# Kernel tuning notes

Measured on AMD Instinct MI355X. Metric: run time of the kernel, lower is better.

## Reference

```python
import jax, jax.numpy as jnp
import numpy as np

N_NODES = 100000
N_EDGES = 3200000
N_GRAPHS = 256
VOCAB = 1500


def gcn_conv(x, edge_index, W, b, n_nodes):
    # x: [N, Fin], edge_index: [2, E] (row=source, col=target)
    h = x @ W  # [N, Fout]
    loops = jnp.arange(n_nodes, dtype=edge_index.dtype)
    row = jnp.concatenate([edge_index[0], loops])
    col = jnp.concatenate([edge_index[1], loops])
    # symmetric normalization with self-loops (PyG GCNConv default)
    deg = jax.ops.segment_sum(jnp.ones_like(col, dtype=h.dtype), col,
                              num_segments=n_nodes)
    dinv = jnp.where(deg > 0, jax.lax.rsqrt(deg), 0.0)
    norm = dinv[row] * dinv[col]  # [E+N]
    msg = h[row] * norm[:, None]  # gather + scale
    out = jax.ops.segment_sum(msg, col, num_segments=n_nodes)  # scatter-add
    return out + b


def setup_inputs() -> dict:
    key = jax.random.key(0)
    k = jax.random.split(key, 8)
    x_ids = jax.random.randint(k[0], (N_NODES,), 0, VOCAB)
    edge_index = jax.random.randint(k[1], (2, N_EDGES), 0, N_NODES)
    batch = jnp.sort(jax.random.randint(k[2], (N_NODES,), 0, N_GRAPHS))
    emb_table = jax.random.normal(k[3], (VOCAB, 16), dtype=jnp.float32)
    W1 = jax.random.normal(k[4], (16, 32), dtype=jnp.float32) * (1.0 / np.sqrt(16))
    b1 = jnp.zeros((32,), dtype=jnp.float32)
    W2 = jax.random.normal(k[5], (32, 41), dtype=jnp.float32) * (1.0 / np.sqrt(32))
    b2 = jnp.zeros((41,), dtype=jnp.float32)
    return {"x_ids": x_ids, "edge_index": edge_index, "batch": batch,
            "emb_table": emb_table, "W1": W1, "b1": b1, "W2": W2, "b2": b2}


def reference(x_ids, edge_index, batch, emb_table, W1, b1, W2, b2):
    x = emb_table[x_ids]                      # embedding lookup [N,16]
    x = gcn_conv(x, edge_index, W1, b1, N_NODES)
    x = jax.nn.relu(x)                        # dropout is identity in eval
    x = gcn_conv(x, edge_index, W2, b2, N_NODES)
    # scatter_add pooling over graphs in batch
    return jax.ops.segment_sum(x, batch, num_segments=N_GRAPHS)  # [G,41]
```

## Files before the change

### kernel.cpp

```cpp
#include <hip/hip_runtime.h>


constexpr int EPB = 16384;
constexpr int BSH = 8;
constexpr int BKTN = 1 << BSH;
constexpr int CAP = 10240;

__device__ inline unsigned short f2bf(float x) {
  unsigned u = __float_as_uint(x);
  u += 0x7FFF + ((u >> 16) & 1);
  return (unsigned short)(u >> 16);
}
__device__ inline float bf2f(unsigned short h) {
  return __uint_as_float((unsigned)h << 16);
}
__device__ inline unsigned pk(float a, float b) {
  return (unsigned)f2bf(a) | ((unsigned)f2bf(b) << 16);
}
__device__ __forceinline__ void add8(float acc[8], uint4 v) {
  acc[0] += bf2f(v.x & 0xFFFF); acc[1] += bf2f(v.x >> 16);
  acc[2] += bf2f(v.y & 0xFFFF); acc[3] += bf2f(v.y >> 16);
  acc[4] += bf2f(v.z & 0xFFFF); acc[5] += bf2f(v.z >> 16);
  acc[6] += bf2f(v.w & 0xFFFF); acc[7] += bf2f(v.w >> 16);
}

__device__ __forceinline__ void gather8(const unsigned short* __restrict__ base,
                                        const int* list, int st, int dg,
                                        float acc[8]) {
  int j = 0;
  for (; j + 4 <= dg; j += 4) {
    int r0 = list[st + j], r1 = list[st + j + 1];
    int r2 = list[st + j + 2], r3 = list[st + j + 3];
    uint4 v0 = *(const uint4*)(base + (size_t)r0 * 16);
    uint4 v1 = *(const uint4*)(base + (size_t)r1 * 16);
    uint4 v2 = *(const uint4*)(base + (size_t)r2 * 16);
    uint4 v3 = *(const uint4*)(base + (size_t)r3 * 16);
    add8(acc, v0); add8(acc, v1); add8(acc, v2); add8(acc, v3);
  }
  for (; j < dg; ++j)
    add8(acc, *(const uint4*)(base + (size_t)list[st + j] * 16));
}

__device__ __forceinline__ int swz(int b, int nblkp) {
  return (b & 7) * (nblkp >> 3) + (b >> 3);
}

__global__ __launch_bounds__(1024) void k_scatter(const int* __restrict__ row,
                                                  const int* __restrict__ col, int E,
                                                  int nbkt, int nblkp,
                                                  int* __restrict__ cursor,
                                                  int* __restrict__ staging) {
  __shared__ int sbuf[EPB];
  __shared__ int cnt[512], sc[512], cur[512], gbase[512];
  int tid = threadIdx.x;
  int lane = tid & 63, wv = tid >> 6;
  int blk = swz(blockIdx.x, nblkp);
  if (tid < 512) cnt[tid] = 0;
  __syncthreads();
  int e0 = blk * EPB, e1 = min(E, e0 + EPB);
  for (int e = e0 + tid; e < e1; e += 1024)
    atomicAdd(&cnt[col[e] >> BSH], 1);
  __syncthreads();
  if (tid < 512) {
    int c = cnt[tid];
    sc[tid] = c;
    gbase[tid] = c ? atomicAdd(&cursor[tid], c) : 0;
  }
  __syncthreads();
  for (int o = 1; o < 512; o <<= 1) {
    int u = (tid < 512 && tid >= o) ? sc[tid - o] : 0;
    __syncthreads();
    if (tid < 512) sc[tid] += u;
    __syncthreads();
  }
  if (tid < 512) { int st = sc[tid] - cnt[tid]; sc[tid] = st; cur[tid] = st; }
  __syncthreads();
  for (int e = e0 + tid; e < e1; e += 1024) {
    int c = col[e];
    int b = c >> BSH;
    int pos = atomicAdd(&cur[b], 1);
    sbuf[pos] = (row[e] << BSH) | (c & (BKTN - 1));
  }
  __syncthreads();
  for (int b = wv; b < nbkt; b += 16) {
    int lbeg = sc[b], lcnt = cnt[b];
    int gb = gbase[b];
    int lim = CAP - gb;
    if (lcnt > lim) lcnt = lim > 0 ? lim : 0;
    int g = b * CAP + gb;
    for (int j = lane; j < lcnt; j += 64)
      staging[g + j] = sbuf[lbeg + j];
  }
}

__global__ __launch_bounds__(512) void k_build(const int* __restrict__ staging,
                                               const int* __restrict__ cursor,
                                               const int* __restrict__ x_ids,
                                               const float* __restrict__ emb,
                                               int N, int nbkt,
                                               int* __restrict__ col_ptr,
                                               int* __restrict__ endp,
                                               float* __restrict__ dinv,
                                               unsigned short* __restrict__ ag1,
                                               int* __restrict__ edge_row) {
  __shared__ int list[CAP];
  __shared__ int cnt[BKTN], sc[BKTN], lcur[BKTN];
  int tid = threadIdx.x, b = blockIdx.x;
  int beg = b * CAP;
  int total = min(cursor[b], CAP);
  int end = beg + total;
  if (tid < BKTN) cnt[tid] = 0;
  __syncthreads();
  for (int i = beg + tid; i < end; i += 512)
    atomicAdd(&cnt[staging[i] & (BKTN - 1)], 1);
  __syncthreads();
  if (tid < BKTN) sc[tid] = cnt[tid];
  __syncthreads();
  for (int o = 1; o < BKTN; o <<= 1) {
    int u = (tid < BKTN && tid >= o) ? sc[tid - o] : 0;
    __syncthreads();
    if (tid < BKTN) sc[tid] += u;
    __syncthreads();
  }
  if (tid < BKTN) {
    int excl = sc[tid] - cnt[tid];
    sc[tid] = excl;
    lcur[tid] = excl;
    int node = (b << BSH) + tid;
    if (node < N) col_ptr[node] = beg + excl;
  }
  if (tid == 0) {
    endp[b] = end;
    if (b == nbkt - 1) col_ptr[N] = end;
  }
  __syncthreads();
  for (int i = beg + tid; i < end; i += 512) {
    int p = staging[i];
    list[atomicAdd(&lcur[p & (BKTN - 1)], 1)] = p >> BSH;
  }
  __syncthreads();
  for (int i = beg + tid; i < end; i += 512)
    edge_row[i] = list[i - beg];
  int nloc = tid >> 1, half = tid & 1;
  int node = (b << BSH) + nloc;
  if (node < N) {
    float d = rsqrtf((float)(cnt[nloc] + 1));
    if (half == 0) dinv[node] = d;
    const float* er = emb + (size_t)x_ids[node] * 16 + half * 8;
    float4 e0 = *(const float4*)(er);
    float4 e1 = *(const float4*)(er + 4);
    uint4 o;
    o.x = pk(e0.x * d, e0.y * d); o.y = pk(e0.z * d, e0.w * d);
    o.z = pk(e1.x * d, e1.y * d); o.w = pk(e1.z * d, e1.w * d);
    *(uint4*)(ag1 + (size_t)node * 16 + half * 8) = o;
  }
}

__global__ __launch_bounds__(512) void k_fuse1(const unsigned short* __restrict__ ag1,
                                               const int* __restrict__ edge_row,
                                               const int* __restrict__ col_ptr,
                                               const int* __restrict__ endp,
                                               const float* __restrict__ dinv,
                                               const float* __restrict__ W1,
                                               const float* __restrict__ b1, int N,
                                               unsigned short* __restrict__ y1g) {
  __shared__ int list[CAP];
  __shared__ float W[512];
  __shared__ float bb[32];
  int tid = threadIdx.x, b = blockIdx.x;
  W[tid] = W1[tid];
  if (tid < 32) bb[tid] = b1[tid];
  int nloc = tid >> 1, half = tid & 1;
  int node = (b << BSH) + nloc;
  bool valid = node < N;
  int beg = b * CAP;
  int end = endp[b];
  int ms = 0, me = 0;
  float acc[8];
  if (valid) {
    ms = col_ptr[node];
    me = (nloc == BKTN - 1) ? end : col_ptr[node + 1];
    uint4 v = *(const uint4*)(ag1 + (size_t)node * 16 + half * 8);
    acc[0] = bf2f(v.x & 0xFFFF); acc[1] = bf2f(v.x >> 16);
    acc[2] = bf2f(v.y & 0xFFFF); acc[3] = bf2f(v.y >> 16);
    acc[4] = bf2f(v.z & 0xFFFF); acc[5] = bf2f(v.z >> 16);
    acc[6] = bf2f(v.w & 0xFFFF); acc[7] = bf2f(v.w >> 16);
  } else {
#pragma unroll
    for (int k = 0; k < 8; ++k) acc[k] = 0.f;
  }
  for (int cbeg = beg; cbeg < end; cbeg += CAP) {
    int cend = min(end, cbeg + CAP);
    __syncthreads();
    for (int i = cbeg + tid; i < cend; i += 512) list[i - cbeg] = edge_row[i];
    __syncthreads();
    if (valid) {
      int st = max(ms, cbeg), en = min(me, cend);
      if (en > st) gather8(ag1 + half * 8, list, st - cbeg, en - st, acc);
    }
  }
  if (!valid) return;
  float d = dinv[node];
  float sx[8], xo[8];
#pragma unroll
  for (int k = 0; k < 8; ++k) sx[k] = acc[k] * d;
#pragma unroll
  for (int k = 0; k < 8; ++k) xo[k] = __shfl_xor(sx[k], 1);
  float x[16];
  if (half == 0) {
#pragma unroll
    for (int k = 0; k < 8; ++k) { x[k] = sx[k]; x[8 + k] = xo[k]; }
  } else {
#pragma unroll
    for (int k = 0; k < 8; ++k) { x[k] = xo[k]; x[8 + k] = sx[k]; }
  }
  int j0 = half * 16;
  float a[16];
#pragma unroll
  for (int j = 0; j < 16; ++j) a[j] = bb[j0 + j];
#pragma unroll
  for (int k = 0; k < 16; ++k) {
    float xv = x[k];
#pragma unroll
    for (int j = 0; j < 16; ++j) a[j] += xv * W[k * 32 + j0 + j];
  }
#pragma unroll
  for (int j = 0; j < 16; ++j) a[j] = fmaxf(a[j], 0.f) * d;
  uint4 o0 = {pk(a[0], a[1]), pk(a[2], a[3]), pk(a[4], a[5]), pk(a[6], a[7])};
  uint4 o1 = {pk(a[8], a[9]), pk(a[10], a[11]), pk(a[12], a[13]), pk(a[14], a[15])};
  unsigned short* yp = y1g + (size_t)half * N * 16 + (size_t)node * 16;
  *(uint4*)(yp) = o0;
  *(uint4*)(yp + 8) = o1;
}

__global__ __launch_bounds__(512) void k_fuse2(const unsigned short* __restrict__ y1g,
                                               const int* __restrict__ edge_row,
                                               const int* __restrict__ col_ptr,
                                               const int* __restrict__ endp,
                                               const float* __restrict__ dinv,
                                               const int* __restrict__ batch, int N,
                                               int nbkt, float* __restrict__ P) {
  __shared__ int list[CAP];
  __shared__ float pool[8 * 16];
  int bx = blockIdx.x;
  int plane = (bx >> 2) & 1;
  int b = (bx >> 3) * 4 + (bx & 3);
  if (b >= nbkt) return;
  const unsigned short* __restrict__ y1p = y1g + (size_t)plane * N * 16;
  int pofs = plane << 4;
  int tid = threadIdx.x;
  int nloc = tid >> 1, half = tid & 1;
  int node = (b << BSH) + nloc;
  bool valid = node < N;
  int beg = b * CAP;
  int end = endp[b];
  int ms = 0, me = 0;
  float acc[8];
  if (valid) {
    ms = col_ptr[node];
    me = (nloc == BKTN - 1) ? end : col_ptr[node + 1];
    uint4 v = *(const uint4*)(y1p + (size_t)node * 16 + half * 8);
    acc[0] = bf2f(v.x & 0xFFFF); acc[1] = bf2f(v.x >> 16);
    acc[2] = bf2f(v.y & 0xFFFF); acc[3] = bf2f(v.y >> 16);
    acc[4] = bf2f(v.z & 0xFFFF); acc[5] = bf2f(v.z >> 16);
    acc[6] = bf2f(v.w & 0xFFFF); acc[7] = bf2f(v.w >> 16);
  } else {
#pragma unroll
    for (int k = 0; k < 8; ++k) acc[k] = 0.f;
  }
  for (int cbeg = beg; cbeg < end; cbeg += CAP) {
    int cend = min(end, cbeg + CAP);
    __syncthreads();
    for (int i = cbeg + tid; i < cend; i += 512) list[i - cbeg] = edge_row[i];
    __syncthreads();
    if (valid) {
      int st = max(ms, cbeg), en = min(me, cend);
      if (en > st) gather8(y1p + half * 8, list, st - cbeg, en - st, acc);
    }
  }
  int myg = -1;
  if (valid) {
    float d = dinv[node];
#pragma unroll
    for (int k = 0; k < 8; ++k) acc[k] *= d;
    myg = batch[node];
  }
  int g0 = batch[b << BSH];
  int g1 = batch[min((b << BSH) + BKTN - 1, N - 1)];
  for (int clo = g0; clo <= g1; clo += 8) {
    for (int j = tid; j < 8 * 16; j += 512) pool[j] = 0.f;
    __syncthreads();
    if (myg >= clo && myg < clo + 8) {
      float* pp = pool + (myg - clo) * 16 + half * 8;
#pragma unroll
      for (int k = 0; k < 8; ++k) atomicAdd(pp + k, acc[k]);
    }
    __syncthreads();
    int ng = min(8, g1 - clo + 1);
    for (int j = tid; j < ng * 16; j += 512)
      atomicAdd(&P[(size_t)(clo + (j >> 4)) * 32 + pofs + (j & 15)], pool[j]);
    __syncthreads();
  }
}

__global__ __launch_bounds__(64) void k_final(const float* __restrict__ P,
                                              const int* __restrict__ batch, int N,
                                              const float* __restrict__ W2,
                                              const float* __restrict__ b2,
                                              float* __restrict__ out) {
  __shared__ float pr[32];
  __shared__ int se[2];
  int g = blockIdx.x, tid = threadIdx.x;
  if (tid < 2) {
    int v = g + tid;
    int lo = 0, hi = N;
    while (lo < hi) {
      int mid = (lo + hi) >> 1;
      if (batch[mid] < v) lo = mid + 1; else hi = mid;
    }
    se[tid] = lo;
  }
  if (tid < 32) pr[tid] = P[(size_t)g * 32 + tid];
  __syncthreads();
  if (tid < 41) {
    float o = (float)(se[1] - se[0]) * b2[tid];
#pragma unroll
    for (int k = 0; k < 32; ++k) o += pr[k] * W2[k * 41 + tid];
    out[(size_t)g * 41 + tid] = o;
  }
}

extern "C" void kernel_launch(void* const* d_in, const int* in_sizes, int n_in,
                              void* d_out, int out_size, void* d_ws, size_t ws_size,
                              hipStream_t stream) {
  const int* x_ids = (const int*)d_in[0];
  const int* edge_index = (const int*)d_in[1];
  const int* batch = (const int*)d_in[2];
  const float* emb = (const float*)d_in[3];
  const float* W1 = (const float*)d_in[4];
  const float* b1 = (const float*)d_in[5];
  const float* W2 = (const float*)d_in[6];
  const float* b2 = (const float*)d_in[7];
  float* out = (float*)d_out;

  const int N = in_sizes[0];
  const int E = in_sizes[1] / 2;
  const int G = out_size / 41;
  const int* row = edge_index;
  const int* col = edge_index + E;

  const int nbkt = (N + BKTN - 1) >> BSH;
  int nblk = (E + EPB - 1) / EPB;
  const int nblkp = (nblk + 7) & ~7;
  const int nbkt4 = (nbkt + 3) & ~3;

  char* ws = (char*)d_ws;
  size_t woff = 0;
  auto alloc = [&](size_t bytes) -> char* {
    char* p = ws + woff;
    woff += (bytes + 255) & ~(size_t)255;
    return p;
  };
  int* staging = (int*)alloc((size_t)nbkt * CAP * 4);
  int* edge_row = (int*)alloc((size_t)nbkt * CAP * 4);
  int* col_ptr = (int*)alloc(((size_t)N + 1) * 4);
  float* dinv = (float*)alloc((size_t)N * 4);
  unsigned short* ag1 = (unsigned short*)alloc((size_t)N * 16 * 2);
  unsigned short* y1g = (unsigned short*)alloc((size_t)N * 32 * 2);
  int* endp = (int*)alloc((size_t)nbkt * 4);
  float* P = (float*)alloc((size_t)G * 32 * 4 + (size_t)nbkt * 4);
  int* cursor = (int*)(P + (size_t)G * 32);
  (void)ws_size; (void)n_in;

  hipMemsetAsync(P, 0, (size_t)G * 32 * 4 + (size_t)nbkt * 4, stream);

  k_scatter<<<nblkp, 1024, 0, stream>>>(row, col, E, nbkt, nblkp, cursor, staging);
  k_build<<<nbkt, 512, 0, stream>>>(staging, cursor, x_ids, emb, N, nbkt,
                                    col_ptr, endp, dinv, ag1, edge_row);
  k_fuse1<<<nbkt, 512, 0, stream>>>(ag1, edge_row, col_ptr, endp, dinv, W1, b1, N, y1g);
  k_fuse2<<<2 * nbkt4, 512, 0, stream>>>(y1g, edge_row, col_ptr, endp, dinv,
                                         batch, N, nbkt, P);
  k_final<<<G, 64, 0, stream>>>(P, batch, N, W2, b2, out);
}
```

Before: 215.0 us.

## Software-pipeline neighbor gathers, vectorize edge-list staging, shrink LDS window

The gather loop is restructured so the next group of four neighbor rows is loaded while the previous group is accumulated, overlapping memory latency with the bf16 adds. Edge-index staging into shared memory now uses int4 vector copies. The shared list window shrinks from 10240 to 8704 entries, which may allow more blocks per CU. Buckets larger than the window now need an extra chunk pass, and the pipelined loop holds more registers live.

Result: faster. 209.9 us (-2.4%).

```diff
diff --git a/kernel.cpp b/kernel.cpp
--- a/kernel.cpp
+++ b/kernel.cpp
@@ -5,6 +5,7 @@
 constexpr int BSH = 8;
 constexpr int BKTN = 1 << BSH;
 constexpr int CAP = 10240;
+constexpr int CAPC = 8704;
 
 __device__ inline unsigned short f2bf(float x) {
   unsigned u = __float_as_uint(x);
@@ -28,17 +29,35 @@
                                         const int* list, int st, int dg,
                                         float acc[8]) {
   int j = 0;
-  for (; j + 4 <= dg; j += 4) {
-    int r0 = list[st + j], r1 = list[st + j + 1];
-    int r2 = list[st + j + 2], r3 = list[st + j + 3];
+  if (dg >= 8) {
+    int r0 = list[st], r1 = list[st + 1], r2 = list[st + 2], r3 = list[st + 3];
     uint4 v0 = *(const uint4*)(base + (size_t)r0 * 16);
     uint4 v1 = *(const uint4*)(base + (size_t)r1 * 16);
     uint4 v2 = *(const uint4*)(base + (size_t)r2 * 16);
     uint4 v3 = *(const uint4*)(base + (size_t)r3 * 16);
+    for (j = 4; j + 4 <= dg; j += 4) {
+      int s0 = list[st + j], s1 = list[st + j + 1];
+      int s2 = list[st + j + 2], s3 = list[st + j + 3];
+      uint4 w0 = *(const uint4*)(base + (size_t)s0 * 16);
+      uint4 w1 = *(const uint4*)(base + (size_t)s1 * 16);
+      uint4 w2 = *(const uint4*)(base + (size_t)s2 * 16);
+      uint4 w3 = *(const uint4*)(base + (size_t)s3 * 16);
+      add8(acc, v0); add8(acc, v1); add8(acc, v2); add8(acc, v3);
+      v0 = w0; v1 = w1; v2 = w2; v3 = w3;
+    }
     add8(acc, v0); add8(acc, v1); add8(acc, v2); add8(acc, v3);
   }
   for (; j < dg; ++j)
     add8(acc, *(const uint4*)(base + (size_t)list[st + j] * 16));
+}
+
+__device__ __forceinline__ void copy_window(int* list, const int* __restrict__ src,
+                                            int n, int tid) {
+  const int4* s4 = (const int4*)src;
+  int4* d4 = (int4*)list;
+  int n4 = n >> 2;
+  for (int i = tid; i < n4; i += 512) d4[i] = s4[i];
+  for (int i = (n4 << 2) + tid; i < n; i += 512) list[i] = src[i];
 }
 
 __device__ __forceinline__ int swz(int b, int nblkp) {
@@ -164,7 +183,7 @@
                                                const float* __restrict__ W1,
                                                const float* __restrict__ b1, int N,
                                                unsigned short* __restrict__ y1g) {
-  __shared__ int list[CAP];
+  __shared__ int list[CAPC];
   __shared__ float W[512];
   __shared__ float bb[32];
   int tid = threadIdx.x, b = blockIdx.x;
@@ -189,10 +208,10 @@
 #pragma unroll
     for (int k = 0; k < 8; ++k) acc[k] = 0.f;
   }
-  for (int cbeg = beg; cbeg < end; cbeg += CAP) {
-    int cend = min(end, cbeg + CAP);
-    __syncthreads();
-    for (int i = cbeg + tid; i < cend; i += 512) list[i - cbeg] = edge_row[i];
+  for (int cbeg = beg; cbeg < end; cbeg += CAPC) {
+    int cend = min(end, cbeg + CAPC);
+    __syncthreads();
+    copy_window(list, edge_row + cbeg, cend - cbeg, tid);
     __syncthreads();
     if (valid) {
       int st = max(ms, cbeg), en = min(me, cend);
@@ -240,7 +259,7 @@
                                                const float* __restrict__ dinv,
                                                const int* __restrict__ batch, int N,
                                                int nbkt, float* __restrict__ P) {
-  __shared__ int list[CAP];
+  __shared__ int list[CAPC];
   __shared__ float pool[8 * 16];
   int bx = blockIdx.x;
   int plane = (bx >> 2) & 1;
@@ -268,10 +287,10 @@
 #pragma unroll
     for (int k = 0; k < 8; ++k) acc[k] = 0.f;
   }
-  for (int cbeg = beg; cbeg < end; cbeg += CAP) {
-    int cend = min(end, cbeg + CAP);
-    __syncthreads();
-    for (int i = cbeg + tid; i < cend; i += 512) list[i - cbeg] = edge_row[i];
+  for (int cbeg = beg; cbeg < end; cbeg += CAPC) {
+    int cend = min(end, cbeg + CAPC);
+    __syncthreads();
+    copy_window(list, edge_row + cbeg, cend - cbeg, tid);
     __syncthreads();
     if (valid) {
       int st = max(ms, cbeg), en = min(me, cend);
```
